# Kernel optimization log

Measured on AMD Instinct MI355X. Metric: run time of the kernel, lower is better.

Reference implementation:

```python
import jax, jax.numpy as jnp
import numpy as np

N_NODES = 100000


def gcn_conv(x, edge_index, W, b):
    """PyG-style GCNConv: x' = D^-1/2 (A+I) D^-1/2 (x W) + b (self-loops added)."""
    n = x.shape[0]
    h = x @ W  # [N, out]
    loop = jnp.arange(n, dtype=edge_index.dtype)
    src = jnp.concatenate([edge_index[0], loop])  # [E+N]
    dst = jnp.concatenate([edge_index[1], loop])
    deg = jax.ops.segment_sum(jnp.ones_like(dst, dtype=h.dtype), dst, num_segments=n)
    dinv = jnp.where(deg > 0, jax.lax.rsqrt(deg), 0.0)
    norm = dinv[src] * dinv[dst]  # [E+N]
    # gather -> scale -> scatter-add aggregation
    out = jax.ops.segment_sum(norm[:, None] * h[src], dst, num_segments=n)
    return out + b


def setup_inputs() -> dict:
    key = jax.random.key(0)
    k1, k2, k3, k4 = jax.random.split(key, 4)
    n, e = N_NODES, 2560000
    x = jax.random.normal(k1, (n, 2), dtype=jnp.float32)
    edge_index = jax.random.randint(k2, (2, e), 0, n, dtype=jnp.int32)
    hidden = 32
    W1 = jax.random.normal(k3, (2, hidden), dtype=jnp.float32) * (1.0 / np.sqrt(2))
    b1 = jnp.zeros((hidden,), dtype=jnp.float32)
    W2 = jax.random.normal(k4, (hidden, 1), dtype=jnp.float32) * (1.0 / np.sqrt(hidden))
    b2 = jnp.zeros((1,), dtype=jnp.float32)
    return {"x": x, "edge_index": edge_index, "W1": W1, "b1": b1, "W2": W2, "b2": b2}


def reference(x, edge_index, W1, b1, W2, b2):
    h = jax.nn.relu(gcn_conv(x, edge_index, W1, b1))
    return gcn_conv(h, edge_index, W2, b2)  # [N, 1]
```

## Files before the change

### kernel.cpp

```cpp
#include <hip/hip_runtime.h>


#define NBMAX 1024
#define NRMAX 32
#define AGG_BLKS 8
#define CHUNK 4096
#define NCHP 640
#define DBITS 12
#define DMASK 4095
#define NOEDGE 0xFFFFFFFFu


__global__ void k_px(const float2* __restrict__ x, const int* __restrict__ pdeg,
                     float* __restrict__ dinv, float2* __restrict__ px, int n) {
    int i = blockIdx.x * blockDim.x + threadIdx.x;
    if (i >= n) return;
    int deg = 1;
#pragma unroll
    for (int b = 0; b < AGG_BLKS; ++b) deg += pdeg[b * n + i];
    float d = rsqrtf((float)deg);
    dinv[i] = d;
    float2 xv = x[i];
    px[i] = make_float2(d * xv.x, d * xv.y);
}

__global__ void k_node(const float2* __restrict__ px, const float2* __restrict__ pP,
                       const float* __restrict__ dinv,
                       const float* __restrict__ W1, const float* __restrict__ b1,
                       const float* __restrict__ W2, float* __restrict__ s, int n) {
    int i = blockIdx.x * blockDim.x + threadIdx.x;
    if (i >= n) return;
    float2 v = px[i];
    float ax = v.x, ay = v.y;
#pragma unroll
    for (int b = 0; b < AGG_BLKS; ++b) {
        float2 p = pP[b * n + i];
        ax += p.x; ay += p.y;
    }
    float d = dinv[i];
    float dot = 0.f;
#pragma unroll
    for (int j = 0; j < 32; ++j) {
        float acc = fmaf(ax, W1[j], ay * W1[32 + j]);
        float h = fmaxf(fmaf(d, acc, b1[j]), 0.f);
        dot = fmaf(h, W2[j], dot);
    }
    s[i] = d * dot;
}

__global__ void k_out(const float* __restrict__ s, const float* __restrict__ ps,
                      const float* __restrict__ dinv, const float* __restrict__ b2,
                      float* __restrict__ out, int n) {
    int i = blockIdx.x * blockDim.x + threadIdx.x;
    if (i >= n) return;
    float acc = s[i];
#pragma unroll
    for (int b = 0; b < AGG_BLKS; ++b) acc += ps[b * n + i];
    out[i] = dinv[i] * acc + b2[0];
}


__device__ __forceinline__ int block_scan_excl(int v, int tid, int* wtot ) {
    int lane = tid & 63, w = tid >> 6;
    int inc = v;
#pragma unroll
    for (int d = 1; d < 64; d <<= 1) {
        int u = __shfl_up(inc, d);
        if (lane >= d) inc += u;
    }
    if (lane == 63) wtot[w] = inc;
    __syncthreads();
    if (w == 0) {
        int t = (lane < 16) ? wtot[lane] : 0;
#pragma unroll
        for (int d = 1; d < 16; d <<= 1) {
            int u = __shfl_up(t, d);
            if (lane >= d) t += u;
        }
        if (lane < 16) wtot[lane] = t;
        if (lane == 15) wtot[16] = t;
    }
    __syncthreads();
    int base = (w > 0) ? wtot[w - 1] : 0;
    return base + inc - v;
}


__global__ void k_cnt(const int* __restrict__ src, const int* __restrict__ dst,
                      int* __restrict__ cnt, int e, int NS, int NB) {
    __shared__ int h[NBMAX];
    for (int t = threadIdx.x; t < NB; t += blockDim.x) h[t] = 0;
    __syncthreads();
    int c0 = blockIdx.x * CHUNK, c1 = min(c0 + CHUNK, e);
    int len = c1 - c0, lq = len >> 2;
    const int4* d4 = (const int4*)(dst + c0);
    const int4* s4 = (const int4*)(src + c0);
    for (int j = threadIdx.x; j < lq; j += blockDim.x) {
        int4 dv = d4[j], sv = s4[j];
        atomicAdd(&h[(dv.x >> DBITS) * NS + (sv.x >> DBITS)], 1);
        atomicAdd(&h[(dv.y >> DBITS) * NS + (sv.y >> DBITS)], 1);
        atomicAdd(&h[(dv.z >> DBITS) * NS + (sv.z >> DBITS)], 1);
        atomicAdd(&h[(dv.w >> DBITS) * NS + (sv.w >> DBITS)], 1);
    }
    if (threadIdx.x == 0)
        for (int i = lq * 4; i < len; ++i)
            atomicAdd(&h[(dst[c0 + i] >> DBITS) * NS + (src[c0 + i] >> DBITS)], 1);
    __syncthreads();
    for (int t = threadIdx.x; t < NB; t += blockDim.x)
        cnt[t * NCHP + blockIdx.x] = h[t];
}

__global__ __launch_bounds__(1024)
void k_scanA(const int* __restrict__ cnt, int* __restrict__ ofs,
             int* __restrict__ tot, int NCH) {
    __shared__ int wtot[17];
    int bin = blockIdx.x, tid = threadIdx.x;
    int v = (tid < NCH) ? cnt[bin * NCHP + tid] : 0;
    int ex = block_scan_excl(v, tid, wtot);
    if (tid < NCH) ofs[bin * NCHP + tid] = ex;
    if (tid == 0) tot[bin] = wtot[16];
}

__global__ __launch_bounds__(1024)
void k_scanB(const int* __restrict__ tot, int* __restrict__ gbin,
             int* __restrict__ rbase, int* __restrict__ rlenp,
             unsigned* __restrict__ packed, int NB, int NS) {
    __shared__ int wtot[17];
    int tid = threadIdx.x;
    int t = (tid < NB) ? tot[tid] : 0;
    int p = (t + 3) & ~3;
    int gb = block_scan_excl(p, tid, wtot);
    int total = wtot[16];
    if (tid < NB) {
        gbin[tid] = gb;
        for (int k = t; k < p; ++k) packed[gb + k] = NOEDGE;
        if ((tid % NS) == 0) rbase[tid / NS] = gb;
    }
    __syncthreads();
    if (tid < NB && (tid % NS) == 0) {
        int r = tid / NS;
        int nxt = (tid + NS < NB) ? gbin[tid + NS] : total;
        rlenp[r] = nxt - gb;
    }
}

__global__ __launch_bounds__(256)
void k_bscatter(const int* __restrict__ src, const int* __restrict__ dst,
                const int* __restrict__ ofs, const int* __restrict__ gbin,
                unsigned* __restrict__ packed, int e, int NS, int NB) {
    __shared__ int h[NBMAX], lofs[NBMAX], curx[NBMAX], gb[NBMAX];
    __shared__ unsigned sbuf[CHUNK];
    __shared__ int dest[CHUNK];
    int blk = blockIdx.x;
    int c0 = blk * CHUNK, c1 = min(c0 + CHUNK, e);
    int len = c1 - c0, lq = len >> 2;
    for (int t = threadIdx.x; t < NB; t += blockDim.x) h[t] = 0;
    __syncthreads();
    const int4* d4 = (const int4*)(dst + c0);
    const int4* s4 = (const int4*)(src + c0);
    for (int j = threadIdx.x; j < lq; j += blockDim.x) {
        int4 dv = d4[j], sv = s4[j];
        atomicAdd(&h[(dv.x >> DBITS) * NS + (sv.x >> DBITS)], 1);
        atomicAdd(&h[(dv.y >> DBITS) * NS + (sv.y >> DBITS)], 1);
        atomicAdd(&h[(dv.z >> DBITS) * NS + (sv.z >> DBITS)], 1);
        atomicAdd(&h[(dv.w >> DBITS) * NS + (sv.w >> DBITS)], 1);
    }
    if (threadIdx.x == 0)
        for (int i = lq * 4; i < len; ++i)
            atomicAdd(&h[(dst[c0 + i] >> DBITS) * NS + (src[c0 + i] >> DBITS)], 1);
    __syncthreads();
    if (threadIdx.x == 0) {
        int acc = 0;
        for (int b = 0; b < NB; ++b) { lofs[b] = acc; acc += h[b]; }
    }
    __syncthreads();
    for (int t = threadIdx.x; t < NB; t += blockDim.x) {
        curx[t] = lofs[t];
        gb[t] = gbin[t] + ofs[t * NCHP + blk];
    }
    __syncthreads();
    for (int j = threadIdx.x; j < lq; j += blockDim.x) {
        int4 dv = d4[j], sv = s4[j];
        {
            int b = (dv.x >> DBITS) * NS + (sv.x >> DBITS);
            int sl = atomicAdd(&curx[b], 1);
            sbuf[sl] = ((unsigned)sv.x << DBITS) | (unsigned)(dv.x & DMASK);
            dest[sl] = gb[b] + (sl - lofs[b]);
        }
        {
            int b = (dv.y >> DBITS) * NS + (sv.y >> DBITS);
            int sl = atomicAdd(&curx[b], 1);
            sbuf[sl] = ((unsigned)sv.y << DBITS) | (unsigned)(dv.y & DMASK);
            dest[sl] = gb[b] + (sl - lofs[b]);
        }
        {
            int b = (dv.z >> DBITS) * NS + (sv.z >> DBITS);
            int sl = atomicAdd(&curx[b], 1);
            sbuf[sl] = ((unsigned)sv.z << DBITS) | (unsigned)(dv.z & DMASK);
            dest[sl] = gb[b] + (sl - lofs[b]);
        }
        {
            int b = (dv.w >> DBITS) * NS + (sv.w >> DBITS);
            int sl = atomicAdd(&curx[b], 1);
            sbuf[sl] = ((unsigned)sv.w << DBITS) | (unsigned)(dv.w & DMASK);
            dest[sl] = gb[b] + (sl - lofs[b]);
        }
    }
    if (threadIdx.x == 0)
        for (int i = lq * 4; i < len; ++i) {
            int d = dst[c0 + i], sx = src[c0 + i];
            int b = (d >> DBITS) * NS + (sx >> DBITS);
            int sl = atomicAdd(&curx[b], 1);
            sbuf[sl] = ((unsigned)sx << DBITS) | (unsigned)(d & DMASK);
            dest[sl] = gb[b] + (sl - lofs[b]);
        }
    __syncthreads();
    for (int t = threadIdx.x; t < len; t += blockDim.x)
        packed[dest[t]] = sbuf[t];
}


__global__ __launch_bounds__(1024, 8)
void k_deg(const unsigned* __restrict__ packed, const int* __restrict__ rbase,
           const int* __restrict__ rlenp, int* __restrict__ pdeg, int n) {
    __shared__ int acc[DMASK + 1];
    int r = blockIdx.y, b = blockIdx.x;
    int rs_r = min(DMASK + 1, n - (r << DBITS));
    for (int t = threadIdx.x; t < rs_r; t += blockDim.x) acc[t] = 0;
    __syncthreads();
    int base = rbase[r], q = rlenp[r] >> 2;
    int qper = (q + AGG_BLKS - 1) / AGG_BLKS;
    int qlo = b * qper, qhi = min(qlo + qper, q);
    const uint4* p4 = (const uint4*)(packed + base);
    for (int j = qlo + threadIdx.x; j < qhi; j += blockDim.x) {
        uint4 v = p4[j];
        if (v.x != NOEDGE) atomicAdd(&acc[v.x & DMASK], 1);
        if (v.y != NOEDGE) atomicAdd(&acc[v.y & DMASK], 1);
        if (v.z != NOEDGE) atomicAdd(&acc[v.z & DMASK], 1);
        if (v.w != NOEDGE) atomicAdd(&acc[v.w & DMASK], 1);
    }
    __syncthreads();
    int nb = b * n + (r << DBITS);
    for (int t = threadIdx.x; t < rs_r; t += blockDim.x) pdeg[nb + t] = acc[t];
}

__global__ __launch_bounds__(1024, 8)
void k_agg1(const unsigned* __restrict__ packed, const int* __restrict__ rbase,
            const int* __restrict__ rlenp, const float2* __restrict__ px,
            float2* __restrict__ pP, int n) {
    __shared__ float acc[2 * (DMASK + 1)];
    int r = blockIdx.y, b = blockIdx.x;
    int rs_r = min(DMASK + 1, n - (r << DBITS));
    for (int t = threadIdx.x; t < 2 * rs_r; t += blockDim.x) acc[t] = 0.f;
    __syncthreads();
    int base = rbase[r], q = rlenp[r] >> 2;
    int qper = (q + AGG_BLKS - 1) / AGG_BLKS;
    int qlo = b * qper, qhi = min(qlo + qper, q);
    const uint4* p4 = (const uint4*)(packed + base);
    int nm1 = n - 1;
    for (int j = qlo + threadIdx.x; j < qhi; j += blockDim.x) {
        uint4 v = p4[j];
        int i0 = min((int)(v.x >> DBITS), nm1);
        int i1 = min((int)(v.y >> DBITS), nm1);
        int i2 = min((int)(v.z >> DBITS), nm1);
        int i3 = min((int)(v.w >> DBITS), nm1);
        float2 g0 = px[i0], g1 = px[i1], g2 = px[i2], g3 = px[i3];
        if (v.x != NOEDGE) { int d0 = (v.x & DMASK) * 2; atomicAdd(&acc[d0], g0.x); atomicAdd(&acc[d0 + 1], g0.y); }
        if (v.y != NOEDGE) { int d1 = (v.y & DMASK) * 2; atomicAdd(&acc[d1], g1.x); atomicAdd(&acc[d1 + 1], g1.y); }
        if (v.z != NOEDGE) { int d2 = (v.z & DMASK) * 2; atomicAdd(&acc[d2], g2.x); atomicAdd(&acc[d2 + 1], g2.y); }
        if (v.w != NOEDGE) { int d3 = (v.w & DMASK) * 2; atomicAdd(&acc[d3], g3.x); atomicAdd(&acc[d3 + 1], g3.y); }
    }
    __syncthreads();
    int nb = b * n + (r << DBITS);
    for (int t = threadIdx.x; t < rs_r; t += blockDim.x)
        pP[nb + t] = make_float2(acc[2 * t], acc[2 * t + 1]);
}

__global__ __launch_bounds__(1024, 8)
void k_agg2(const unsigned* __restrict__ packed, const int* __restrict__ rbase,
            const int* __restrict__ rlenp, const float* __restrict__ s,
            float* __restrict__ ps, int n) {
    __shared__ float acc[DMASK + 1];
    int r = blockIdx.y, b = blockIdx.x;
    int rs_r = min(DMASK + 1, n - (r << DBITS));
    for (int t = threadIdx.x; t < rs_r; t += blockDim.x) acc[t] = 0.f;
    __syncthreads();
    int base = rbase[r], q = rlenp[r] >> 2;
    int qper = (q + AGG_BLKS - 1) / AGG_BLKS;
    int qlo = b * qper, qhi = min(qlo + qper, q);
    const uint4* p4 = (const uint4*)(packed + base);
    int nm1 = n - 1;
    for (int j = qlo + threadIdx.x; j < qhi; j += blockDim.x) {
        uint4 v = p4[j];
        int i0 = min((int)(v.x >> DBITS), nm1);
        int i1 = min((int)(v.y >> DBITS), nm1);
        int i2 = min((int)(v.z >> DBITS), nm1);
        int i3 = min((int)(v.w >> DBITS), nm1);
        float g0 = s[i0], g1 = s[i1], g2 = s[i2], g3 = s[i3];
        if (v.x != NOEDGE) atomicAdd(&acc[v.x & DMASK], g0);
        if (v.y != NOEDGE) atomicAdd(&acc[v.y & DMASK], g1);
        if (v.z != NOEDGE) atomicAdd(&acc[v.z & DMASK], g2);
        if (v.w != NOEDGE) atomicAdd(&acc[v.w & DMASK], g3);
    }
    __syncthreads();
    int nb = b * n + (r << DBITS);
    for (int t = threadIdx.x; t < rs_r; t += blockDim.x) ps[nb + t] = acc[t];
}


__global__ void f_zero(int* __restrict__ ideg, float2* __restrict__ P, int n) {
    int i = blockIdx.x * blockDim.x + threadIdx.x;
    if (i < n) { ideg[i] = 0; P[i] = make_float2(0.f, 0.f); }
}
__global__ void f_count(const int* __restrict__ dst, int* __restrict__ ideg, int e) {
    int i = blockIdx.x * blockDim.x + threadIdx.x;
    if (i < e) atomicAdd(&ideg[dst[i]], 1);
}
__global__ void f_px(const float2* __restrict__ x, const int* __restrict__ ideg,
                     float* __restrict__ dinv, float2* __restrict__ px, int n) {
    int i = blockIdx.x * blockDim.x + threadIdx.x;
    if (i >= n) return;
    float d = rsqrtf((float)(1 + ideg[i]));
    dinv[i] = d;
    float2 xv = x[i];
    px[i] = make_float2(d * xv.x, d * xv.y);
}
__global__ void f_scatter_px(const int* __restrict__ src, const int* __restrict__ dst,
                             const float2* __restrict__ px, float* __restrict__ Pf, int e) {
    int i = blockIdx.x * blockDim.x + threadIdx.x;
    if (i >= e) return;
    int sidx = src[i], d = dst[i];
    float2 v = px[sidx];
    atomicAdd(&Pf[2 * d], v.x);
    atomicAdd(&Pf[2 * d + 1], v.y);
}
__global__ void f_node(const float2* __restrict__ px, const float2* __restrict__ P,
                       const float* __restrict__ dinv,
                       const float* __restrict__ W1, const float* __restrict__ b1,
                       const float* __restrict__ W2,
                       float* __restrict__ s, float* __restrict__ S, int n) {
    int i = blockIdx.x * blockDim.x + threadIdx.x;
    if (i >= n) return;
    float d = dinv[i];
    float2 v = px[i], p = P[i];
    float ax = v.x + p.x, ay = v.y + p.y;
    float dot = 0.f;
#pragma unroll
    for (int j = 0; j < 32; ++j) {
        float acc = fmaf(ax, W1[j], ay * W1[32 + j]);
        float h = fmaxf(fmaf(d, acc, b1[j]), 0.f);
        dot = fmaf(h, W2[j], dot);
    }
    float sv = d * dot;
    s[i] = sv;
    S[i] = sv;
}
__global__ void f_scatter_s(const int* __restrict__ src, const int* __restrict__ dst,
                            const float* __restrict__ s, float* __restrict__ S, int e) {
    int i = blockIdx.x * blockDim.x + threadIdx.x;
    if (i < e) atomicAdd(&S[dst[i]], s[src[i]]);
}
__global__ void f_out(const float* __restrict__ S, const float* __restrict__ dinv,
                      const float* __restrict__ b2, float* __restrict__ out, int n) {
    int i = blockIdx.x * blockDim.x + threadIdx.x;
    if (i < n) out[i] = dinv[i] * S[i] + b2[0];
}


extern "C" void kernel_launch(void* const* d_in, const int* in_sizes, int n_in,
                              void* d_out, int out_size, void* d_ws, size_t ws_size,
                              hipStream_t stream) {
    const float* x  = (const float*)d_in[0];
    const int*   ei = (const int*)d_in[1];
    const float* W1 = (const float*)d_in[2];
    const float* b1 = (const float*)d_in[3];
    const float* W2 = (const float*)d_in[4];
    const float* b2 = (const float*)d_in[5];
    float* out = (float*)d_out;

    int n = in_sizes[0] / 2;
    int e = in_sizes[1] / 2;
    const int* src = ei;
    const int* dst = ei + e;
    int NR  = (n + DMASK) >> DBITS;
    int NS  = NR;
    int NB  = NR * NS;
    int NCH = (e + CHUNK - 1) / CHUNK;

    char* ws = (char*)d_ws;
    auto align = [](size_t v) { return (v + 255) & ~(size_t)255; };
    size_t off = 0;
    float*  dinv = (float*) (ws + off); off = align(off + (size_t)n * 4);
    float2* px   = (float2*)(ws + off); off = align(off + (size_t)n * 8);
    float*  s    = (float*) (ws + off); off = align(off + (size_t)n * 4);
    int*    pdeg = (int*)   (ws + off); off = align(off + (size_t)AGG_BLKS * n * 4);
    float2* pP   = (float2*)(ws + off); off = align(off + (size_t)AGG_BLKS * n * 8);
    float*  ps   = (float*) (ws + off); off = align(off + (size_t)AGG_BLKS * n * 4);
    int*    rbase = (int*)(ws + off); off = align(off + NRMAX * 4);
    int*    rlenp = (int*)(ws + off); off = align(off + NRMAX * 4);
    int*    gbin  = (int*)(ws + off); off = align(off + NBMAX * 4);
    int*    tot   = (int*)(ws + off); off = align(off + NBMAX * 4);
    int*    cnt   = (int*)(ws + off); off = align(off + (size_t)NBMAX * NCHP * 4);
    int*    ofs   = (int*)(ws + off); off = align(off + (size_t)NBMAX * NCHP * 4);
    unsigned* packed = (unsigned*)(ws + off);
    size_t need = off + (size_t)(e + 4 * NBMAX) * 4;

    const int B = 256;
    int gn = (n + B - 1) / B, ge = (e + B - 1) / B;

    bool fast = (need <= ws_size) && (NB <= NBMAX) && (NCH <= NCHP) && (NR <= NRMAX);

    if (fast) {
        dim3 ag(AGG_BLKS, NR);
        k_cnt     <<<NCH, B, 0, stream>>>(src, dst, cnt, e, NS, NB);
        k_scanA   <<<NB, 1024, 0, stream>>>(cnt, ofs, tot, NCH);
        k_scanB   <<<1, 1024, 0, stream>>>(tot, gbin, rbase, rlenp, packed, NB, NS);
        k_bscatter<<<NCH, B, 0, stream>>>(src, dst, ofs, gbin, packed, e, NS, NB);
        k_deg     <<<ag, 1024, 0, stream>>>(packed, rbase, rlenp, pdeg, n);
        k_px      <<<gn, B, 0, stream>>>((const float2*)x, pdeg, dinv, px, n);
        k_agg1    <<<ag, 1024, 0, stream>>>(packed, rbase, rlenp, px, pP, n);
        k_node    <<<gn, B, 0, stream>>>(px, pP, dinv, W1, b1, W2, s, n);
        k_agg2    <<<ag, 1024, 0, stream>>>(packed, rbase, rlenp, s, ps, n);
        k_out     <<<gn, B, 0, stream>>>(s, ps, dinv, b2, out, n);
    } else {
        int*   ideg = pdeg;
        float2* P   = pP;
        float* S    = ps;
        f_zero      <<<gn, B, 0, stream>>>(ideg, P, n);
        f_count     <<<ge, B, 0, stream>>>(dst, ideg, e);
        f_px        <<<gn, B, 0, stream>>>((const float2*)x, ideg, dinv, px, n);
        f_scatter_px<<<ge, B, 0, stream>>>(src, dst, px, (float*)P, e);
        f_node      <<<gn, B, 0, stream>>>(px, P, dinv, W1, b1, W2, s, S, n);
        f_scatter_s <<<ge, B, 0, stream>>>(src, dst, s, S, e);
        f_out       <<<gn, B, 0, stream>>>(S, dinv, b2, out, n);
    }
}
```

Measured before the change: 111.2 us.

## Fuse per-node epilogues into aggregation kernels via last-block counters; reuse bin counts

Removes the separate k_px, k_node, k_out and k_scanB launches. The last block to finish each row (detected with an atomic done counter after a threadfence) now performs the per-node epilogue work. k_cnt also writes a transposed per-chunk histogram, so k_bscatter no longer recounts edges with shared atomics and instead does a parallel block scan of the stored counts at 1024 threads. This cuts four launches and a redundant pass over the edges, but the epilogue now runs serially inside a single block per row, and a memset is added to reset the counters.

```diff
diff --git a/kernel.cpp b/kernel.cpp
--- a/kernel.cpp
+++ b/kernel.cpp
@@ -11,55 +11,6 @@
 #define NOEDGE 0xFFFFFFFFu
 
 
-__global__ void k_px(const float2* __restrict__ x, const int* __restrict__ pdeg,
-                     float* __restrict__ dinv, float2* __restrict__ px, int n) {
-    int i = blockIdx.x * blockDim.x + threadIdx.x;
-    if (i >= n) return;
-    int deg = 1;
-#pragma unroll
-    for (int b = 0; b < AGG_BLKS; ++b) deg += pdeg[b * n + i];
-    float d = rsqrtf((float)deg);
-    dinv[i] = d;
-    float2 xv = x[i];
-    px[i] = make_float2(d * xv.x, d * xv.y);
-}
-
-__global__ void k_node(const float2* __restrict__ px, const float2* __restrict__ pP,
-                       const float* __restrict__ dinv,
-                       const float* __restrict__ W1, const float* __restrict__ b1,
-                       const float* __restrict__ W2, float* __restrict__ s, int n) {
-    int i = blockIdx.x * blockDim.x + threadIdx.x;
-    if (i >= n) return;
-    float2 v = px[i];
-    float ax = v.x, ay = v.y;
-#pragma unroll
-    for (int b = 0; b < AGG_BLKS; ++b) {
-        float2 p = pP[b * n + i];
-        ax += p.x; ay += p.y;
-    }
-    float d = dinv[i];
-    float dot = 0.f;
-#pragma unroll
-    for (int j = 0; j < 32; ++j) {
-        float acc = fmaf(ax, W1[j], ay * W1[32 + j]);
-        float h = fmaxf(fmaf(d, acc, b1[j]), 0.f);
-        dot = fmaf(h, W2[j], dot);
-    }
-    s[i] = d * dot;
-}
-
-__global__ void k_out(const float* __restrict__ s, const float* __restrict__ ps,
-                      const float* __restrict__ dinv, const float* __restrict__ b2,
-                      float* __restrict__ out, int n) {
-    int i = blockIdx.x * blockDim.x + threadIdx.x;
-    if (i >= n) return;
-    float acc = s[i];
-#pragma unroll
-    for (int b = 0; b < AGG_BLKS; ++b) acc += ps[b * n + i];
-    out[i] = dinv[i] * acc + b2[0];
-}
-
-
 __device__ __forceinline__ int block_scan_excl(int v, int tid, int* wtot ) {
     int lane = tid & 63, w = tid >> 6;
     int inc = v;
@@ -87,7 +38,8 @@
 
 
 __global__ void k_cnt(const int* __restrict__ src, const int* __restrict__ dst,
-                      int* __restrict__ cnt, int e, int NS, int NB) {
+                      int* __restrict__ cnt, int* __restrict__ cntT,
+                      int e, int NS, int NB) {
     __shared__ int h[NBMAX];
     for (int t = threadIdx.x; t < NB; t += blockDim.x) h[t] = 0;
     __syncthreads();
@@ -106,133 +58,129 @@
         for (int i = lq * 4; i < len; ++i)
             atomicAdd(&h[(dst[c0 + i] >> DBITS) * NS + (src[c0 + i] >> DBITS)], 1);
     __syncthreads();
-    for (int t = threadIdx.x; t < NB; t += blockDim.x)
-        cnt[t * NCHP + blockIdx.x] = h[t];
+    for (int t = threadIdx.x; t < NB; t += blockDim.x) {
+        int v = h[t];
+        cnt[t * NCHP + blockIdx.x] = v;
+        cntT[blockIdx.x * NBMAX + t] = v;
+    }
 }
 
 __global__ __launch_bounds__(1024)
 void k_scanA(const int* __restrict__ cnt, int* __restrict__ ofs,
-             int* __restrict__ tot, int NCH) {
+             int* __restrict__ tot, int* __restrict__ doneA,
+             int* __restrict__ gbin, int* __restrict__ rbase, int* __restrict__ rlenp,
+             unsigned* __restrict__ packed, int NB, int NS, int NCH) {
     __shared__ int wtot[17];
+    __shared__ int lastflag;
     int bin = blockIdx.x, tid = threadIdx.x;
     int v = (tid < NCH) ? cnt[bin * NCHP + tid] : 0;
     int ex = block_scan_excl(v, tid, wtot);
     if (tid < NCH) ofs[bin * NCHP + tid] = ex;
     if (tid == 0) tot[bin] = wtot[16];
-}
-
-__global__ __launch_bounds__(1024)
-void k_scanB(const int* __restrict__ tot, int* __restrict__ gbin,
-             int* __restrict__ rbase, int* __restrict__ rlenp,
-             unsigned* __restrict__ packed, int NB, int NS) {
-    __shared__ int wtot[17];
-    int tid = threadIdx.x;
+    __syncthreads();
+    if (tid == 0) {
+        __threadfence();
+        lastflag = (atomicAdd(doneA, 1) == (int)gridDim.x - 1) ? 1 : 0;
+    }
+    __syncthreads();
+    if (!lastflag) return;
     int t = (tid < NB) ? tot[tid] : 0;
     int p = (t + 3) & ~3;
+    __syncthreads();
     int gb = block_scan_excl(p, tid, wtot);
-    int total = wtot[16];
+    int totalp = wtot[16];
     if (tid < NB) {
         gbin[tid] = gb;
         for (int k = t; k < p; ++k) packed[gb + k] = NOEDGE;
-        if ((tid % NS) == 0) rbase[tid / NS] = gb;
     }
     __syncthreads();
     if (tid < NB && (tid % NS) == 0) {
         int r = tid / NS;
-        int nxt = (tid + NS < NB) ? gbin[tid + NS] : total;
+        rbase[r] = gb;
+        int nxt = (tid + NS < NB) ? gbin[tid + NS] : totalp;
         rlenp[r] = nxt - gb;
     }
 }
 
-__global__ __launch_bounds__(256)
+__global__ __launch_bounds__(1024)
 void k_bscatter(const int* __restrict__ src, const int* __restrict__ dst,
-                const int* __restrict__ ofs, const int* __restrict__ gbin,
-                unsigned* __restrict__ packed, int e, int NS, int NB) {
-    __shared__ int h[NBMAX], lofs[NBMAX], curx[NBMAX], gb[NBMAX];
+                const int* __restrict__ cntT, const int* __restrict__ ofs,
+                const int* __restrict__ gbin, unsigned* __restrict__ packed,
+                int e, int NS, int NB) {
+    __shared__ int lofs[NBMAX], curx[NBMAX], gb[NBMAX];
     __shared__ unsigned sbuf[CHUNK];
     __shared__ int dest[CHUNK];
-    int blk = blockIdx.x;
+    __shared__ int wtot[17];
+    int blk = blockIdx.x, tid = threadIdx.x;
     int c0 = blk * CHUNK, c1 = min(c0 + CHUNK, e);
     int len = c1 - c0, lq = len >> 2;
-    for (int t = threadIdx.x; t < NB; t += blockDim.x) h[t] = 0;
+    int hv = (tid < NB) ? cntT[blk * NBMAX + tid] : 0;
+    int lo = block_scan_excl(hv, tid, wtot);
+    if (tid < NB) {
+        lofs[tid] = lo;
+        curx[tid] = lo;
+        gb[tid] = gbin[tid] + ofs[tid * NCHP + blk] - lo;
+    }
     __syncthreads();
     const int4* d4 = (const int4*)(dst + c0);
     const int4* s4 = (const int4*)(src + c0);
-    for (int j = threadIdx.x; j < lq; j += blockDim.x) {
-        int4 dv = d4[j], sv = s4[j];
-        atomicAdd(&h[(dv.x >> DBITS) * NS + (sv.x >> DBITS)], 1);
-        atomicAdd(&h[(dv.y >> DBITS) * NS + (sv.y >> DBITS)], 1);
-        atomicAdd(&h[(dv.z >> DBITS) * NS + (sv.z >> DBITS)], 1);
-        atomicAdd(&h[(dv.w >> DBITS) * NS + (sv.w >> DBITS)], 1);
-    }
-    if (threadIdx.x == 0)
-        for (int i = lq * 4; i < len; ++i)
-            atomicAdd(&h[(dst[c0 + i] >> DBITS) * NS + (src[c0 + i] >> DBITS)], 1);
-    __syncthreads();
-    if (threadIdx.x == 0) {
-        int acc = 0;
-        for (int b = 0; b < NB; ++b) { lofs[b] = acc; acc += h[b]; }
-    }
-    __syncthreads();
-    for (int t = threadIdx.x; t < NB; t += blockDim.x) {
-        curx[t] = lofs[t];
-        gb[t] = gbin[t] + ofs[t * NCHP + blk];
-    }
-    __syncthreads();
-    for (int j = threadIdx.x; j < lq; j += blockDim.x) {
+    for (int j = tid; j < lq; j += blockDim.x) {
         int4 dv = d4[j], sv = s4[j];
         {
             int b = (dv.x >> DBITS) * NS + (sv.x >> DBITS);
             int sl = atomicAdd(&curx[b], 1);
             sbuf[sl] = ((unsigned)sv.x << DBITS) | (unsigned)(dv.x & DMASK);
-            dest[sl] = gb[b] + (sl - lofs[b]);
+            dest[sl] = gb[b] + sl;
         }
         {
             int b = (dv.y >> DBITS) * NS + (sv.y >> DBITS);
             int sl = atomicAdd(&curx[b], 1);
             sbuf[sl] = ((unsigned)sv.y << DBITS) | (unsigned)(dv.y & DMASK);
-            dest[sl] = gb[b] + (sl - lofs[b]);
+            dest[sl] = gb[b] + sl;
         }
         {
             int b = (dv.z >> DBITS) * NS + (sv.z >> DBITS);
             int sl = atomicAdd(&curx[b], 1);
             sbuf[sl] = ((unsigned)sv.z << DBITS) | (unsigned)(dv.z & DMASK);
-            dest[sl] = gb[b] + (sl - lofs[b]);
+            dest[sl] = gb[b] + sl;
         }
         {
             int b = (dv.w >> DBITS) * NS + (sv.w >> DBITS);
             int sl = atomicAdd(&curx[b], 1);
             sbuf[sl] = ((unsigned)sv.w << DBITS) | (unsigned)(dv.w & DMASK);
-            dest[sl] = gb[b] + (sl - lofs[b]);
-        }
-    }
-    if (threadIdx.x == 0)
+            dest[sl] = gb[b] + sl;
+        }
+    }
+    if (tid == 0)
         for (int i = lq * 4; i < len; ++i) {
             int d = dst[c0 + i], sx = src[c0 + i];
             int b = (d >> DBITS) * NS + (sx >> DBITS);
             int sl = atomicAdd(&curx[b], 1);
             sbuf[sl] = ((unsigned)sx << DBITS) | (unsigned)(d & DMASK);
-            dest[sl] = gb[b] + (sl - lofs[b]);
-        }
-    __syncthreads();
-    for (int t = threadIdx.x; t < len; t += blockDim.x)
+            dest[sl] = gb[b] + sl;
+        }
+    __syncthreads();
+    for (int t = tid; t < len; t += blockDim.x)
         packed[dest[t]] = sbuf[t];
 }
 
 
 __global__ __launch_bounds__(1024, 8)
-void k_deg(const unsigned* __restrict__ packed, const int* __restrict__ rbase,
-           const int* __restrict__ rlenp, int* __restrict__ pdeg, int n) {
+void k_degpx(const unsigned* __restrict__ packed, const int* __restrict__ rbase,
+             const int* __restrict__ rlenp, int* __restrict__ pdeg,
+             int* __restrict__ done_deg, const float2* __restrict__ x,
+             float* __restrict__ dinv, float2* __restrict__ px, int n) {
     __shared__ int acc[DMASK + 1];
-    int r = blockIdx.y, b = blockIdx.x;
+    __shared__ int lastflag;
+    int r = blockIdx.y, b = blockIdx.x, tid = threadIdx.x;
     int rs_r = min(DMASK + 1, n - (r << DBITS));
-    for (int t = threadIdx.x; t < rs_r; t += blockDim.x) acc[t] = 0;
+    for (int t = tid; t < rs_r; t += blockDim.x) acc[t] = 0;
     __syncthreads();
     int base = rbase[r], q = rlenp[r] >> 2;
     int qper = (q + AGG_BLKS - 1) / AGG_BLKS;
     int qlo = b * qper, qhi = min(qlo + qper, q);
     const uint4* p4 = (const uint4*)(packed + base);
-    for (int j = qlo + threadIdx.x; j < qhi; j += blockDim.x) {
+    for (int j = qlo + tid; j < qhi; j += blockDim.x) {
         uint4 v = p4[j];
         if (v.x != NOEDGE) atomicAdd(&acc[v.x & DMASK], 1);
         if (v.y != NOEDGE) atomicAdd(&acc[v.y & DMASK], 1);
@@ -241,24 +189,46 @@
     }
     __syncthreads();
     int nb = b * n + (r << DBITS);
-    for (int t = threadIdx.x; t < rs_r; t += blockDim.x) pdeg[nb + t] = acc[t];
-}
-
-__global__ __launch_bounds__(1024, 8)
-void k_agg1(const unsigned* __restrict__ packed, const int* __restrict__ rbase,
-            const int* __restrict__ rlenp, const float2* __restrict__ px,
-            float2* __restrict__ pP, int n) {
+    for (int t = tid; t < rs_r; t += blockDim.x) pdeg[nb + t] = acc[t];
+    __syncthreads();
+    if (tid == 0) {
+        __threadfence();
+        lastflag = (atomicAdd(&done_deg[r], 1) == (int)gridDim.x - 1) ? 1 : 0;
+    }
+    __syncthreads();
+    if (!lastflag) return;
+    int nbase = r << DBITS;
+    for (int t = tid; t < rs_r; t += blockDim.x) {
+        int i = nbase + t;
+        int deg = 1;
+#pragma unroll
+        for (int bb = 0; bb < AGG_BLKS; ++bb) deg += pdeg[bb * n + i];
+        float d = rsqrtf((float)deg);
+        dinv[i] = d;
+        float2 xv = x[i];
+        px[i] = make_float2(d * xv.x, d * xv.y);
+    }
+}
+
+__global__ __launch_bounds__(1024, 4)
+void k_agg1n(const unsigned* __restrict__ packed, const int* __restrict__ rbase,
+             const int* __restrict__ rlenp, const float2* __restrict__ px,
+             float2* __restrict__ pP, int* __restrict__ done_a1,
+             const float* __restrict__ dinv, const float* __restrict__ W1,
+             const float* __restrict__ b1, const float* __restrict__ W2,
+             float* __restrict__ s, int n) {
     __shared__ float acc[2 * (DMASK + 1)];
-    int r = blockIdx.y, b = blockIdx.x;
+    __shared__ int lastflag;
+    int r = blockIdx.y, b = blockIdx.x, tid = threadIdx.x;
     int rs_r = min(DMASK + 1, n - (r << DBITS));
-    for (int t = threadIdx.x; t < 2 * rs_r; t += blockDim.x) acc[t] = 0.f;
+    for (int t = tid; t < 2 * rs_r; t += blockDim.x) acc[t] = 0.f;
     __syncthreads();
     int base = rbase[r], q = rlenp[r] >> 2;
     int qper = (q + AGG_BLKS - 1) / AGG_BLKS;
     int qlo = b * qper, qhi = min(qlo + qper, q);
     const uint4* p4 = (const uint4*)(packed + base);
     int nm1 = n - 1;
-    for (int j = qlo + threadIdx.x; j < qhi; j += blockDim.x) {
+    for (int j = qlo + tid; j < qhi; j += blockDim.x) {
         uint4 v = p4[j];
         int i0 = min((int)(v.x >> DBITS), nm1);
         int i1 = min((int)(v.y >> DBITS), nm1);
@@ -272,25 +242,55 @@
     }
     __syncthreads();
     int nb = b * n + (r << DBITS);
-    for (int t = threadIdx.x; t < rs_r; t += blockDim.x)
+    for (int t = tid; t < rs_r; t += blockDim.x)
         pP[nb + t] = make_float2(acc[2 * t], acc[2 * t + 1]);
+    __syncthreads();
+    if (tid == 0) {
+        __threadfence();
+        lastflag = (atomicAdd(&done_a1[r], 1) == (int)gridDim.x - 1) ? 1 : 0;
+    }
+    __syncthreads();
+    if (!lastflag) return;
+    int nbase = r << DBITS;
+    for (int t = tid; t < rs_r; t += blockDim.x) {
+        int i = nbase + t;
+        float2 v = px[i];
+        float ax = v.x, ay = v.y;
+#pragma unroll
+        for (int bb = 0; bb < AGG_BLKS; ++bb) {
+            float2 p = pP[bb * n + i];
+            ax += p.x; ay += p.y;
+        }
+        float d = dinv[i];
+        float dot = 0.f;
+#pragma unroll
+        for (int j = 0; j < 32; ++j) {
+            float a2 = fmaf(ax, W1[j], ay * W1[32 + j]);
+            float hh = fmaxf(fmaf(d, a2, b1[j]), 0.f);
+            dot = fmaf(hh, W2[j], dot);
+        }
+        s[i] = d * dot;
+    }
 }
 
 __global__ __launch_bounds__(1024, 8)
-void k_agg2(const unsigned* __restrict__ packed, const int* __restrict__ rbase,
-            const int* __restrict__ rlenp, const float* __restrict__ s,
-            float* __restrict__ ps, int n) {
+void k_agg2o(const unsigned* __restrict__ packed, const int* __restrict__ rbase,
+             const int* __restrict__ rlenp, const float* __restrict__ s,
+             float* __restrict__ ps, int* __restrict__ done_a2,
+             const float* __restrict__ dinv, const float* __restrict__ b2,
+             float* __restrict__ out, int n) {
     __shared__ float acc[DMASK + 1];
-    int r = blockIdx.y, b = blockIdx.x;
+    __shared__ int lastflag;
+    int r = blockIdx.y, b = blockIdx.x, tid = threadIdx.x;
     int rs_r = min(DMASK + 1, n - (r << DBITS));
-    for (int t = threadIdx.x; t < rs_r; t += blockDim.x) acc[t] = 0.f;
+    for (int t = tid; t < rs_r; t += blockDim.x) acc[t] = 0.f;
     __syncthreads();
     int base = rbase[r], q = rlenp[r] >> 2;
     int qper = (q + AGG_BLKS - 1) / AGG_BLKS;
     int qlo = b * qper, qhi = min(qlo + qper, q);
     const uint4* p4 = (const uint4*)(packed + base);
     int nm1 = n - 1;
-    for (int j = qlo + threadIdx.x; j < qhi; j += blockDim.x) {
+    for (int j = qlo + tid; j < qhi; j += blockDim.x) {
         uint4 v = p4[j];
         int i0 = min((int)(v.x >> DBITS), nm1);
         int i1 = min((int)(v.y >> DBITS), nm1);
@@ -304,7 +304,23 @@
     }
     __syncthreads();
     int nb = b * n + (r << DBITS);
-    for (int t = threadIdx.x; t < rs_r; t += blockDim.x) ps[nb + t] = acc[t];
+    for (int t = tid; t < rs_r; t += blockDim.x) ps[nb + t] = acc[t];
+    __syncthreads();
+    if (tid == 0) {
+        __threadfence();
+        lastflag = (atomicAdd(&done_a2[r], 1) == (int)gridDim.x - 1) ? 1 : 0;
+    }
+    __syncthreads();
+    if (!lastflag) return;
+    int nbase = r << DBITS;
+    float bias = b2[0];
+    for (int t = tid; t < rs_r; t += blockDim.x) {
+        int i = nbase + t;
+        float a2 = s[i];
+#pragma unroll
+        for (int bb = 0; bb < AGG_BLKS; ++bb) a2 += ps[bb * n + i];
+        out[i] = dinv[i] * a2 + bias;
+    }
 }
 
 
@@ -400,7 +416,13 @@
     int*    rlenp = (int*)(ws + off); off = align(off + NRMAX * 4);
     int*    gbin  = (int*)(ws + off); off = align(off + NBMAX * 4);
     int*    tot   = (int*)(ws + off); off = align(off + NBMAX * 4);
+    int*    ctrl  = (int*)(ws + off); off = align(off + 512);
+    int*    doneA    = ctrl;
+    int*    done_deg = ctrl + 16;
+    int*    done_a1  = ctrl + 16 + NRMAX;
+    int*    done_a2  = ctrl + 16 + 2 * NRMAX;
     int*    cnt   = (int*)(ws + off); off = align(off + (size_t)NBMAX * NCHP * 4);
+    int*    cntT  = (int*)(ws + off); off = align(off + (size_t)NCHP * NBMAX * 4);
     int*    ofs   = (int*)(ws + off); off = align(off + (size_t)NBMAX * NCHP * 4);
     unsigned* packed = (unsigned*)(ws + off);
     size_t need = off + (size_t)(e + 4 * NBMAX) * 4;
@@ -412,16 +434,17 @@
 
     if (fast) {
         dim3 ag(AGG_BLKS, NR);
-        k_cnt     <<<NCH, B, 0, stream>>>(src, dst, cnt, e, NS, NB);
-        k_scanA   <<<NB, 1024, 0, stream>>>(cnt, ofs, tot, NCH);
-        k_scanB   <<<1, 1024, 0, stream>>>(tot, gbin, rbase, rlenp, packed, NB, NS);
-        k_bscatter<<<NCH, B, 0, stream>>>(src, dst, ofs, gbin, packed, e, NS, NB);
-        k_deg     <<<ag, 1024, 0, stream>>>(packed, rbase, rlenp, pdeg, n);
-        k_px      <<<gn, B, 0, stream>>>((const float2*)x, pdeg, dinv, px, n);
-        k_agg1    <<<ag, 1024, 0, stream>>>(packed, rbase, rlenp, px, pP, n);
-        k_node    <<<gn, B, 0, stream>>>(px, pP, dinv, W1, b1, W2, s, n);
-        k_agg2    <<<ag, 1024, 0, stream>>>(packed, rbase, rlenp, s, ps, n);
-        k_out     <<<gn, B, 0, stream>>>(s, ps, dinv, b2, out, n);
+        hipMemsetAsync(ctrl, 0, 512, stream);
+        k_cnt     <<<NCH, B, 0, stream>>>(src, dst, cnt, cntT, e, NS, NB);
+        k_scanA   <<<NB, 1024, 0, stream>>>(cnt, ofs, tot, doneA, gbin, rbase, rlenp,
+                                            packed, NB, NS, NCH);
+        k_bscatter<<<NCH, 1024, 0, stream>>>(src, dst, cntT, ofs, gbin, packed, e, NS, NB);
+        k_degpx   <<<ag, 1024, 0, stream>>>(packed, rbase, rlenp, pdeg, done_deg,
+                                            (const float2*)x, dinv, px, n);
+        k_agg1n   <<<ag, 1024, 0, stream>>>(packed, rbase, rlenp, px, pP, done_a1,
+                                            dinv, W1, b1, W2, s, n);
+        k_agg2o   <<<ag, 1024, 0, stream>>>(packed, rbase, rlenp, s, ps, done_a2,
+                                            dinv, b2, out, n);
     } else {
         int*   ideg = pdeg;
         float2* P   = pP;
```

Measured after the change: 150.3 us. 35.1% more time.

## Reuse scanned chunk counts in bucket scatter instead of re-histogramming

Applied to the files above, without the earlier changes.

The bucket-scatter kernel no longer rebuilds the per-chunk histogram. It derives per-bin counts from adjacent exclusive-scan offsets, which are now stored in place in a transposed count array, and does a block scan in place of a serial single-thread prefix sum. This removes a full second pass over src/dst and the shared atomics in k_bscatter. The kernel now runs with 1024 threads per block, and the aggregation split across blocks doubles from 8 to 16 per row. In exchange, the per-node reduction kernels now sum twice as many partial buffers.

```diff
diff --git a/kernel.cpp b/kernel.cpp
--- a/kernel.cpp
+++ b/kernel.cpp
@@ -3,7 +3,7 @@
 
 #define NBMAX 1024
 #define NRMAX 32
-#define AGG_BLKS 8
+#define AGG_BLKS 16
 #define CHUNK 4096
 #define NCHP 640
 #define DBITS 12
@@ -11,6 +11,32 @@
 #define NOEDGE 0xFFFFFFFFu
 
 
+__device__ __forceinline__ int block_scan_excl(int v, int tid, int* wtot ) {
+    int lane = tid & 63, w = tid >> 6;
+    int inc = v;
+#pragma unroll
+    for (int d = 1; d < 64; d <<= 1) {
+        int u = __shfl_up(inc, d);
+        if (lane >= d) inc += u;
+    }
+    if (lane == 63) wtot[w] = inc;
+    __syncthreads();
+    if (w == 0) {
+        int t = (lane < 16) ? wtot[lane] : 0;
+#pragma unroll
+        for (int d = 1; d < 16; d <<= 1) {
+            int u = __shfl_up(t, d);
+            if (lane >= d) t += u;
+        }
+        if (lane < 16) wtot[lane] = t;
+        if (lane == 15) wtot[16] = t;
+    }
+    __syncthreads();
+    int base = (w > 0) ? wtot[w - 1] : 0;
+    return base + inc - v;
+}
+
+
 __global__ void k_px(const float2* __restrict__ x, const int* __restrict__ pdeg,
                      float* __restrict__ dinv, float2* __restrict__ px, int n) {
     int i = blockIdx.x * blockDim.x + threadIdx.x;
@@ -60,34 +86,8 @@
 }
 
 
-__device__ __forceinline__ int block_scan_excl(int v, int tid, int* wtot ) {
-    int lane = tid & 63, w = tid >> 6;
-    int inc = v;
-#pragma unroll
-    for (int d = 1; d < 64; d <<= 1) {
-        int u = __shfl_up(inc, d);
-        if (lane >= d) inc += u;
-    }
-    if (lane == 63) wtot[w] = inc;
-    __syncthreads();
-    if (w == 0) {
-        int t = (lane < 16) ? wtot[lane] : 0;
-#pragma unroll
-        for (int d = 1; d < 16; d <<= 1) {
-            int u = __shfl_up(t, d);
-            if (lane >= d) t += u;
-        }
-        if (lane < 16) wtot[lane] = t;
-        if (lane == 15) wtot[16] = t;
-    }
-    __syncthreads();
-    int base = (w > 0) ? wtot[w - 1] : 0;
-    return base + inc - v;
-}
-
-
 __global__ void k_cnt(const int* __restrict__ src, const int* __restrict__ dst,
-                      int* __restrict__ cnt, int e, int NS, int NB) {
+                      int* __restrict__ cntT, int e, int NS, int NB) {
     __shared__ int h[NBMAX];
     for (int t = threadIdx.x; t < NB; t += blockDim.x) h[t] = 0;
     __syncthreads();
@@ -107,17 +107,16 @@
             atomicAdd(&h[(dst[c0 + i] >> DBITS) * NS + (src[c0 + i] >> DBITS)], 1);
     __syncthreads();
     for (int t = threadIdx.x; t < NB; t += blockDim.x)
-        cnt[t * NCHP + blockIdx.x] = h[t];
+        cntT[blockIdx.x * NBMAX + t] = h[t];
 }
 
 __global__ __launch_bounds__(1024)
-void k_scanA(const int* __restrict__ cnt, int* __restrict__ ofs,
-             int* __restrict__ tot, int NCH) {
+void k_scanA(int* __restrict__ cntT, int* __restrict__ tot, int NCH) {
     __shared__ int wtot[17];
     int bin = blockIdx.x, tid = threadIdx.x;
-    int v = (tid < NCH) ? cnt[bin * NCHP + tid] : 0;
+    int v = (tid < NCH) ? cntT[tid * NBMAX + bin] : 0;
     int ex = block_scan_excl(v, tid, wtot);
-    if (tid < NCH) ofs[bin * NCHP + tid] = ex;
+    if (tid < NCH) cntT[tid * NBMAX + bin] = ex;
     if (tid == 0) tot[bin] = wtot[16];
 }
 
@@ -130,92 +129,83 @@
     int t = (tid < NB) ? tot[tid] : 0;
     int p = (t + 3) & ~3;
     int gb = block_scan_excl(p, tid, wtot);
-    int total = wtot[16];
+    int totalp = wtot[16];
     if (tid < NB) {
         gbin[tid] = gb;
         for (int k = t; k < p; ++k) packed[gb + k] = NOEDGE;
-        if ((tid % NS) == 0) rbase[tid / NS] = gb;
     }
     __syncthreads();
     if (tid < NB && (tid % NS) == 0) {
         int r = tid / NS;
-        int nxt = (tid + NS < NB) ? gbin[tid + NS] : total;
+        rbase[r] = gb;
+        int nxt = (tid + NS < NB) ? gbin[tid + NS] : totalp;
         rlenp[r] = nxt - gb;
     }
 }
 
-__global__ __launch_bounds__(256)
+__global__ __launch_bounds__(1024)
 void k_bscatter(const int* __restrict__ src, const int* __restrict__ dst,
-                const int* __restrict__ ofs, const int* __restrict__ gbin,
-                unsigned* __restrict__ packed, int e, int NS, int NB) {
-    __shared__ int h[NBMAX], lofs[NBMAX], curx[NBMAX], gb[NBMAX];
+                const int* __restrict__ ofsT, const int* __restrict__ tot,
+                const int* __restrict__ gbin, unsigned* __restrict__ packed,
+                int e, int NS, int NB, int NCH) {
+    __shared__ int curx[NBMAX], gba[NBMAX];
     __shared__ unsigned sbuf[CHUNK];
     __shared__ int dest[CHUNK];
-    int blk = blockIdx.x;
+    __shared__ int wtot[17];
+    int blk = blockIdx.x, tid = threadIdx.x;
     int c0 = blk * CHUNK, c1 = min(c0 + CHUNK, e);
     int len = c1 - c0, lq = len >> 2;
-    for (int t = threadIdx.x; t < NB; t += blockDim.x) h[t] = 0;
+    int cur = 0, hv = 0;
+    if (tid < NB) {
+        cur = ofsT[blk * NBMAX + tid];
+        int nxt = (blk + 1 < NCH) ? ofsT[(blk + 1) * NBMAX + tid] : tot[tid];
+        hv = nxt - cur;
+    }
+    int lo = block_scan_excl(hv, tid, wtot);
+    if (tid < NB) {
+        curx[tid] = lo;
+        gba[tid] = gbin[tid] + cur - lo;
+    }
     __syncthreads();
     const int4* d4 = (const int4*)(dst + c0);
     const int4* s4 = (const int4*)(src + c0);
-    for (int j = threadIdx.x; j < lq; j += blockDim.x) {
-        int4 dv = d4[j], sv = s4[j];
-        atomicAdd(&h[(dv.x >> DBITS) * NS + (sv.x >> DBITS)], 1);
-        atomicAdd(&h[(dv.y >> DBITS) * NS + (sv.y >> DBITS)], 1);
-        atomicAdd(&h[(dv.z >> DBITS) * NS + (sv.z >> DBITS)], 1);
-        atomicAdd(&h[(dv.w >> DBITS) * NS + (sv.w >> DBITS)], 1);
-    }
-    if (threadIdx.x == 0)
-        for (int i = lq * 4; i < len; ++i)
-            atomicAdd(&h[(dst[c0 + i] >> DBITS) * NS + (src[c0 + i] >> DBITS)], 1);
-    __syncthreads();
-    if (threadIdx.x == 0) {
-        int acc = 0;
-        for (int b = 0; b < NB; ++b) { lofs[b] = acc; acc += h[b]; }
-    }
-    __syncthreads();
-    for (int t = threadIdx.x; t < NB; t += blockDim.x) {
-        curx[t] = lofs[t];
-        gb[t] = gbin[t] + ofs[t * NCHP + blk];
-    }
-    __syncthreads();
-    for (int j = threadIdx.x; j < lq; j += blockDim.x) {
+    for (int j = tid; j < lq; j += blockDim.x) {
         int4 dv = d4[j], sv = s4[j];
         {
             int b = (dv.x >> DBITS) * NS + (sv.x >> DBITS);
             int sl = atomicAdd(&curx[b], 1);
             sbuf[sl] = ((unsigned)sv.x << DBITS) | (unsigned)(dv.x & DMASK);
-            dest[sl] = gb[b] + (sl - lofs[b]);
+            dest[sl] = gba[b] + sl;
         }
         {
             int b = (dv.y >> DBITS) * NS + (sv.y >> DBITS);
             int sl = atomicAdd(&curx[b], 1);
             sbuf[sl] = ((unsigned)sv.y << DBITS) | (unsigned)(dv.y & DMASK);
-            dest[sl] = gb[b] + (sl - lofs[b]);
+            dest[sl] = gba[b] + sl;
         }
         {
             int b = (dv.z >> DBITS) * NS + (sv.z >> DBITS);
             int sl = atomicAdd(&curx[b], 1);
             sbuf[sl] = ((unsigned)sv.z << DBITS) | (unsigned)(dv.z & DMASK);
-            dest[sl] = gb[b] + (sl - lofs[b]);
+            dest[sl] = gba[b] + sl;
         }
         {
             int b = (dv.w >> DBITS) * NS + (sv.w >> DBITS);
             int sl = atomicAdd(&curx[b], 1);
             sbuf[sl] = ((unsigned)sv.w << DBITS) | (unsigned)(dv.w & DMASK);
-            dest[sl] = gb[b] + (sl - lofs[b]);
-        }
-    }
-    if (threadIdx.x == 0)
+            dest[sl] = gba[b] + sl;
+        }
+    }
+    if (tid == 0)
         for (int i = lq * 4; i < len; ++i) {
             int d = dst[c0 + i], sx = src[c0 + i];
             int b = (d >> DBITS) * NS + (sx >> DBITS);
             int sl = atomicAdd(&curx[b], 1);
             sbuf[sl] = ((unsigned)sx << DBITS) | (unsigned)(d & DMASK);
-            dest[sl] = gb[b] + (sl - lofs[b]);
-        }
-    __syncthreads();
-    for (int t = threadIdx.x; t < len; t += blockDim.x)
+            dest[sl] = gba[b] + sl;
+        }
+    __syncthreads();
+    for (int t = tid; t < len; t += blockDim.x)
         packed[dest[t]] = sbuf[t];
 }
 
@@ -229,7 +219,7 @@
     for (int t = threadIdx.x; t < rs_r; t += blockDim.x) acc[t] = 0;
     __syncthreads();
     int base = rbase[r], q = rlenp[r] >> 2;
-    int qper = (q + AGG_BLKS - 1) / AGG_BLKS;
+    int qper = (q + gridDim.x - 1) / gridDim.x;
     int qlo = b * qper, qhi = min(qlo + qper, q);
     const uint4* p4 = (const uint4*)(packed + base);
     for (int j = qlo + threadIdx.x; j < qhi; j += blockDim.x) {
@@ -254,7 +244,7 @@
     for (int t = threadIdx.x; t < 2 * rs_r; t += blockDim.x) acc[t] = 0.f;
     __syncthreads();
     int base = rbase[r], q = rlenp[r] >> 2;
-    int qper = (q + AGG_BLKS - 1) / AGG_BLKS;
+    int qper = (q + gridDim.x - 1) / gridDim.x;
     int qlo = b * qper, qhi = min(qlo + qper, q);
     const uint4* p4 = (const uint4*)(packed + base);
     int nm1 = n - 1;
@@ -286,7 +276,7 @@
     for (int t = threadIdx.x; t < rs_r; t += blockDim.x) acc[t] = 0.f;
     __syncthreads();
     int base = rbase[r], q = rlenp[r] >> 2;
-    int qper = (q + AGG_BLKS - 1) / AGG_BLKS;
+    int qper = (q + gridDim.x - 1) / gridDim.x;
     int qlo = b * qper, qhi = min(qlo + qper, q);
     const uint4* p4 = (const uint4*)(packed + base);
     int nm1 = n - 1;
@@ -400,8 +390,7 @@
     int*    rlenp = (int*)(ws + off); off = align(off + NRMAX * 4);
     int*    gbin  = (int*)(ws + off); off = align(off + NBMAX * 4);
     int*    tot   = (int*)(ws + off); off = align(off + NBMAX * 4);
-    int*    cnt   = (int*)(ws + off); off = align(off + (size_t)NBMAX * NCHP * 4);
-    int*    ofs   = (int*)(ws + off); off = align(off + (size_t)NBMAX * NCHP * 4);
+    int*    cntT  = (int*)(ws + off); off = align(off + (size_t)NCHP * NBMAX * 4);
     unsigned* packed = (unsigned*)(ws + off);
     size_t need = off + (size_t)(e + 4 * NBMAX) * 4;
 
@@ -412,10 +401,10 @@
 
     if (fast) {
         dim3 ag(AGG_BLKS, NR);
-        k_cnt     <<<NCH, B, 0, stream>>>(src, dst, cnt, e, NS, NB);
-        k_scanA   <<<NB, 1024, 0, stream>>>(cnt, ofs, tot, NCH);
+        k_cnt     <<<NCH, B, 0, stream>>>(src, dst, cntT, e, NS, NB);
+        k_scanA   <<<NB, 1024, 0, stream>>>(cntT, tot, NCH);
         k_scanB   <<<1, 1024, 0, stream>>>(tot, gbin, rbase, rlenp, packed, NB, NS);
-        k_bscatter<<<NCH, B, 0, stream>>>(src, dst, ofs, gbin, packed, e, NS, NB);
+        k_bscatter<<<NCH, 1024, 0, stream>>>(src, dst, cntT, tot, gbin, packed, e, NS, NB, NCH);
         k_deg     <<<ag, 1024, 0, stream>>>(packed, rbase, rlenp, pdeg, n);
         k_px      <<<gn, B, 0, stream>>>((const float2*)x, pdeg, dinv, px, n);
         k_agg1    <<<ag, 1024, 0, stream>>>(packed, rbase, rlenp, px, pP, n);
```

Result: no change. 110.2 us (-0.8%).
